# Optimization experiments

Measured on AMD Instinct MI355X. Metric: run time of the kernel, lower is better.

Reference implementation:

```python
import jax, jax.numpy as jnp
import numpy as np

# --- fixed OpenCV filter kernels ---
# cv2.getGaussianKernel(3, 1): exp(-(i-1)^2/2), normalized -> [0.27407, 0.45186, 0.27407]
_g = np.exp(-((np.arange(3) - 1.0) ** 2) / 2.0)
GAUSS_1D = (_g / _g.sum()).astype(np.float32)
# cv2 Sobel/Laplacian ksize=9 separable parts (unnormalized, as cv2.Laplacian uses):
#   smoothing = binomial row C(8,k); second derivative = C(6,k) conv [1,-2,1]
SMOOTH_9 = np.array([1, 8, 28, 56, 70, 56, 28, 8, 1], dtype=np.float32)
D2_9 = np.array([1, 4, 4, -4, -10, -4, 4, 4, 1], dtype=np.float32)


def _depthwise_conv(x, k2d):
    """Depthwise 2D correlation with BORDER_REFLECT_101 padding (cv2 default).

    x: [N,H,W,C] float, k2d: [kh,kw] float (symmetric, so corr == conv)."""
    C = x.shape[-1]
    rh, rw = k2d.shape[0] // 2, k2d.shape[1] // 2
    # jnp 'reflect' == OpenCV BORDER_REFLECT_101 (edge pixel not duplicated)
    xp = jnp.pad(x, ((0, 0), (rh, rh), (rw, rw), (0, 0)), mode='reflect')
    k = jnp.broadcast_to(k2d[:, :, None, None], (k2d.shape[0], k2d.shape[1], 1, C))
    return jax.lax.conv_general_dilated(
        xp, k, window_strides=(1, 1), padding='VALID',
        dimension_numbers=('NHWC', 'HWIO', 'NHWC'),
        feature_group_count=C)


def setup_inputs() -> dict:
    key = jax.random.key(0)
    # uint8-range image batch, as the original layer feeds uint8 data to OpenCV
    x = jax.random.uniform(key, (32, 512, 512, 3), dtype=jnp.float32) * 255.0
    return {"x": x}


def reference(x) -> jnp.ndarray:
    g = jnp.asarray(GAUSS_1D)
    blur = _depthwise_conv(x, jnp.outer(g, g))  # GaussianBlur(ksize=3, sigma=1)
    lap_k = jnp.asarray(np.outer(SMOOTH_9, D2_9) + np.outer(D2_9, SMOOTH_9))
    lap = _depthwise_conv(blur, lap_k) + 1.0  # delta = 1
    # CV_8UC1 destination depth -> saturate to [0, 255]
    return jnp.clip(lap, 0.0, 255.0)
```

## Files before the change

### kernel.cpp

```cpp
#include <hip/hip_runtime.h>


#define TH 16
#define TW 32
#define BF ((TW+8)*3)
#define PH (TH+2)
#define VW 124
#define PW 108
#define HIMG 512
#define WIMG 512
#define ROWF (WIMG*3)

#define OFF_VQ 3120
#define SM_TOTAL 5352

__device__ __forceinline__ int reflect101(int i, int n) {
    i = (i < 0) ? -i : i;
    return (i >= n) ? (2 * n - 2 - i) : i;
}

__device__ __forceinline__ float4 fma4(float s, const float4& a, const float4& b) {
    return make_float4(fmaf(s, a.x, b.x), fmaf(s, a.y, b.y),
                       fmaf(s, a.z, b.z), fmaf(s, a.w, b.w));
}

__device__ __forceinline__ float c6dot(float f0, float f1, float f2, float f3,
                                       float f4, float f5, float f6) {
    return fmaf(20.f, f3, fmaf(6.f, f1 + f5, fmaf(15.f, f2 + f4, f0 + f6)));
}

__device__ __forceinline__ float4 g3(const float4& a, const float4& b, const float4& c,
                                     float G0, float G1) {
    return make_float4(G0 * (a.x + c.x) + G1 * b.x,
                       G0 * (a.y + c.y) + G1 * b.y,
                       G0 * (a.z + c.z) + G1 * b.z,
                       G0 * (a.w + c.w) + G1 * b.w);
}

#define U0 0.27406862f
#define U1 2.09627447f
#define U2 7.09627447f
#define U3 13.90372553f
#define U4 17.25931382f

__global__ __launch_bounds__(256, 6)
void log_fused(const float* __restrict__ x, float* __restrict__ out) {
    __shared__ __align__(16) float smem[SM_TOTAL];
    float* const hblur = smem;
    float* const P     = smem;
    float* const vq    = smem + OFF_VQ;

    const int tid  = threadIdx.x;
    const int col0 = blockIdx.x * TW;
    const int row0 = blockIdx.y * TH;
    const int n    = blockIdx.z;

    const int R0    = max(0, row0 - 5);
    const int R1    = min(HIMG - 1, row0 + TH + 4);
    const int nrows = R1 - R0 + 1;

    const float G0 = 0.2740686190f, G1 = 0.4518627620f;

    if (tid < PH)
        *(float4*)&vq[tid * VW + 120] = make_float4(0.f, 0.f, 0.f, 0.f);

    const bool edgecol = (col0 == 0) || (col0 + TW == WIMG);
    if (!edgecol) {
        if (tid < 240) {
            const int cg = tid % 30;
            const int rg = tid / 30;
            const float* xb = x + ((size_t)n * HIMG + (size_t)(R0 + rg)) * ROWF
                                + (3 * (col0 - 4) + 4 * cg - 4);
            float* hb = hblur + rg * BF + 4 * cg;
            for (int r = rg; r < nrows; r += 8, xb += 8 * ROWF, hb += 8 * BF) {
                const float4 a = *(const float4*)(xb);
                const float4 b = *(const float4*)(xb + 4);
                const float4 c = *(const float4*)(xb + 8);
                float4 o;
                o.x = G0 * (a.y + b.w) + G1 * b.x;
                o.y = G0 * (a.z + c.x) + G1 * b.y;
                o.z = G0 * (a.w + c.y) + G1 * b.z;
                o.w = G0 * (b.x + c.z) + G1 * b.w;
                *(float4*)hb = o;
            }
        }
    } else {
        if (tid < 240) {
            const int lc  = tid % BF;
            const int rg  = tid / BF;
            const int lcp = lc / 3;
            const int ch  = lc - 3 * lcp;
            const int gc  = reflect101(col0 - 4 + lcp, WIMG);
            const int xm  = reflect101(gc - 1, WIMG) * 3 + ch;
            const int x0  = gc * 3 + ch;
            const int xp  = reflect101(gc + 1, WIMG) * 3 + ch;
            const float* xr = x + ((size_t)n * HIMG + (size_t)(R0 + rg)) * ROWF;
            for (int r = rg; r < nrows; r += 2, xr += 2 * ROWF) {
                hblur[r * BF + lc] = G0 * (xr[xm] + xr[xp]) + G1 * xr[x0];
            }
        }
    }
    __syncthreads();

    if (row0 != 0 && row0 != HIMG - TH) {
        if (tid < 180) {
            const int rg = tid / 30;
            const int qc = tid % 30;
            const float U9k[9] = {U0, U1, U2, U3, U4, U3, U2, U1, U0};
            const float* hb = hblur + (3 * rg) * BF + 4 * qc;
            float4 a0 = make_float4(0.f, 0.f, 0.f, 0.f), a1 = a0, a2 = a0;
            #pragma unroll
            for (int j = 0; j < 11; ++j) {
                const float4 w = *(const float4*)(hb + j * BF);
                if (j <= 8)           a0 = fma4(U9k[j],     w, a0);
                if (j >= 1 && j <= 9) a1 = fma4(U9k[j - 1], w, a1);
                if (j >= 2)           a2 = fma4(U9k[j - 2], w, a2);
            }
            float* vp = vq + (3 * rg) * VW + 4 * qc;
            *(float4*)vp            = a0;
            *(float4*)(vp + VW)     = a1;
            *(float4*)(vp + 2 * VW) = a2;
        }
    } else {
        const float C6k[7] = {1.f, 6.f, 15.f, 20.f, 15.f, 6.f, 1.f};
        for (int g = tid; g < PH * 30; g += 256) {
            const int r  = g / 30;
            const int qc = g - r * 30;
            const int gb = row0 - 4 + r;
            float4 acc = make_float4(0.f, 0.f, 0.f, 0.f);
            #pragma unroll
            for (int k = 0; k < 7; ++k) {
                const int y  = reflect101(gb + k, HIMG);
                const int ym = reflect101(y - 1, HIMG) - R0;
                const int yp = reflect101(y + 1, HIMG) - R0;
                const float4 a = *(const float4*)&hblur[ym * BF + 4 * qc];
                const float4 b = *(const float4*)&hblur[(y - R0) * BF + 4 * qc];
                const float4 c = *(const float4*)&hblur[yp * BF + 4 * qc];
                acc = fma4(C6k[k], g3(a, b, c, G0, G1), acc);
            }
            *(float4*)&vq[r * VW + 4 * qc] = acc;
        }
    }
    __syncthreads();

    if (tid < PH * 13) {
        const int qp = tid % 13;
        const int r  = tid / 13;
        const float* v = vq + r * VW + 8 * qp;
        float f[28];
        #pragma unroll
        for (int c = 0; c < 7; ++c) {
            const float4 w = *(const float4*)(v + 4 * c);
            f[4*c+0] = w.x; f[4*c+1] = w.y; f[4*c+2] = w.z; f[4*c+3] = w.w;
        }
        float p[8];
        #pragma unroll
        for (int j = 0; j < 8; ++j)
            p[j] = c6dot(f[j], f[j+3], f[j+6], f[j+9], f[j+12], f[j+15], f[j+18]);
        float* pr = P + r * PW + 8 * qp;
        *(float4*)pr       = make_float4(p[0], p[1], p[2], p[3]);
        *(float4*)(pr + 4) = make_float4(p[4], p[5], p[6], p[7]);
    }
    __syncthreads();

    float* const outn = out + (size_t)n * HIMG * ROWF;
    if (tid < TH * 12) {
        const int qp = tid % 12;
        const int i  = tid / 12;
        const int o  = qp * 8;
        const float* pt = P + i * PW + o;
        const float* pm = pt + PW;
        const float* pb = pm + PW;
        float t[16], m[12], b[16];
        #pragma unroll
        for (int q = 0; q < 4; ++q) {
            const float4 vt = *(const float4*)(pt + 4 * q);
            t[4*q+0] = vt.x; t[4*q+1] = vt.y; t[4*q+2] = vt.z; t[4*q+3] = vt.w;
            const float4 vb = *(const float4*)(pb + 4 * q);
            b[4*q+0] = vb.x; b[4*q+1] = vb.y; b[4*q+2] = vb.z; b[4*q+3] = vb.w;
        }
        #pragma unroll
        for (int q = 0; q < 3; ++q) {
            const float4 vm = *(const float4*)(pm + 4 * q);
            m[4*q+0] = vm.x; m[4*q+1] = vm.y; m[4*q+2] = vm.z; m[4*q+3] = vm.w;
        }
        float o8[8];
        #pragma unroll
        for (int j = 0; j < 8; ++j) {
            const float c = m[j + 3];
            const float s = (t[j] - c) + (t[j + 6] - c) + (b[j] - c) + (b[j + 6] - c);
            const float v = fmaf(2.f, s, 1.f);
            o8[j] = fminf(fmaxf(v, 0.f), 255.f);
        }
        float* op = outn + (size_t)(row0 + i) * ROWF + (size_t)(col0 * 3 + o);
        *(float4*)op       = make_float4(o8[0], o8[1], o8[2], o8[3]);
        *(float4*)(op + 4) = make_float4(o8[4], o8[5], o8[6], o8[7]);
    }
}

extern "C" void kernel_launch(void* const* d_in, const int* in_sizes, int n_in,
                              void* d_out, int out_size, void* d_ws, size_t ws_size,
                              hipStream_t stream) {
    const float* x = (const float*)d_in[0];
    float* outp = (float*)d_out;
    const int nimg = in_sizes[0] / (HIMG * WIMG * 3);
    dim3 grid(WIMG / TW, HIMG / TH, nimg);
    log_fused<<<grid, dim3(256, 1, 1), 0, stream>>>(x, outp);
}
```

Before: 221.7 us.

## Double tile height, software-pipeline row loads, vectorize edge-column blur path

```diff
diff --git a/kernel.cpp b/kernel.cpp
--- a/kernel.cpp
+++ b/kernel.cpp
@@ -1,9 +1,9 @@
 #include <hip/hip_runtime.h>
 
 
-#define TH 16
+#define TH 32
 #define TW 32
-#define BF ((TW+8)*3)
+#define BF 120
 #define PH (TH+2)
 #define VW 124
 #define PW 108
@@ -11,8 +11,8 @@
 #define WIMG 512
 #define ROWF (WIMG*3)
 
-#define OFF_VQ 3120
-#define SM_TOTAL 5352
+#define OFF_VQ 5040
+#define SM_TOTAL 9256
 
 __device__ __forceinline__ int reflect101(int i, int n) {
     i = (i < 0) ? -i : i;
@@ -27,14 +27,6 @@
 __device__ __forceinline__ float c6dot(float f0, float f1, float f2, float f3,
                                        float f4, float f5, float f6) {
     return fmaf(20.f, f3, fmaf(6.f, f1 + f5, fmaf(15.f, f2 + f4, f0 + f6)));
-}
-
-__device__ __forceinline__ float4 g3(const float4& a, const float4& b, const float4& c,
-                                     float G0, float G1) {
-    return make_float4(G0 * (a.x + c.x) + G1 * b.x,
-                       G0 * (a.y + c.y) + G1 * b.y,
-                       G0 * (a.z + c.z) + G1 * b.z,
-                       G0 * (a.w + c.w) + G1 * b.w);
 }
 
 #define U0 0.27406862f
@@ -43,7 +35,7 @@
 #define U3 13.90372553f
 #define U4 17.25931382f
 
-__global__ __launch_bounds__(256, 6)
+__global__ __launch_bounds__(256, 4)
 void log_fused(const float* __restrict__ x, float* __restrict__ out) {
     __shared__ __align__(16) float smem[SM_TOTAL];
     float* const hblur = smem;
@@ -54,6 +46,7 @@
     const int col0 = blockIdx.x * TW;
     const int row0 = blockIdx.y * TH;
     const int n    = blockIdx.z;
+    const float* const xi = x + (size_t)n * HIMG * ROWF;
 
     const int R0    = max(0, row0 - 5);
     const int R1    = min(HIMG - 1, row0 + TH + 4);
@@ -69,45 +62,79 @@
         if (tid < 240) {
             const int cg = tid % 30;
             const int rg = tid / 30;
-            const float* xb = x + ((size_t)n * HIMG + (size_t)(R0 + rg)) * ROWF
-                                + (3 * (col0 - 4) + 4 * cg - 4);
+            const float* xp = xi + (size_t)(R0 + rg) * ROWF
+                                 + (3 * (col0 - 4) + 4 * cg - 4);
             float* hb = hblur + rg * BF + 4 * cg;
-            for (int r = rg; r < nrows; r += 8, xb += 8 * ROWF, hb += 8 * BF) {
-                const float4 a = *(const float4*)(xb);
-                const float4 b = *(const float4*)(xb + 4);
-                const float4 c = *(const float4*)(xb + 8);
+            int r = rg;
+            float4 A0 = *(const float4*)(xp);
+            float4 A1 = *(const float4*)(xp + 4);
+            float4 A2 = *(const float4*)(xp + 8);
+            while (true) {
+                const int rn = r + 8;
+                const bool hn = rn < nrows;
+                const float* xn = xp + 8 * ROWF;
+                float4 B0, B1, B2;
+                if (hn) {
+                    B0 = *(const float4*)(xn);
+                    B1 = *(const float4*)(xn + 4);
+                    B2 = *(const float4*)(xn + 8);
+                }
                 float4 o;
+                o.x = G0 * (A0.y + A1.w) + G1 * A1.x;
+                o.y = G0 * (A0.z + A2.x) + G1 * A1.y;
+                o.z = G0 * (A0.w + A2.y) + G1 * A1.z;
+                o.w = G0 * (A1.x + A2.z) + G1 * A1.w;
+                *(float4*)hb = o;
+                if (!hn) break;
+                A0 = B0; A1 = B1; A2 = B2;
+                r = rn; xp = xn; hb += 8 * BF;
+            }
+        }
+    } else {
+        for (int e = tid; e < nrows * 30; e += 256) {
+            const int row = e / 30;
+            const int q   = e - row * 30;
+            const float* xr = xi + (size_t)(R0 + row) * ROWF;
+            const int lcpmin = (4 * q) / 3;
+            const int lcpmax = (4 * q + 3) / 3;
+            const bool safe = (col0 - 5 + lcpmin >= 0) && (col0 - 3 + lcpmax <= WIMG - 1);
+            float4 o;
+            if (safe) {
+                const float* p = xr + (3 * col0 - 16 + 4 * q);
+                const float4 a = *(const float4*)(p);
+                const float4 b = *(const float4*)(p + 4);
+                const float4 c = *(const float4*)(p + 8);
                 o.x = G0 * (a.y + b.w) + G1 * b.x;
                 o.y = G0 * (a.z + c.x) + G1 * b.y;
                 o.z = G0 * (a.w + c.y) + G1 * b.z;
                 o.w = G0 * (b.x + c.z) + G1 * b.w;
-                *(float4*)hb = o;
-            }
-        }
-    } else {
-        if (tid < 240) {
-            const int lc  = tid % BF;
-            const int rg  = tid / BF;
-            const int lcp = lc / 3;
-            const int ch  = lc - 3 * lcp;
-            const int gc  = reflect101(col0 - 4 + lcp, WIMG);
-            const int xm  = reflect101(gc - 1, WIMG) * 3 + ch;
-            const int x0  = gc * 3 + ch;
-            const int xp  = reflect101(gc + 1, WIMG) * 3 + ch;
-            const float* xr = x + ((size_t)n * HIMG + (size_t)(R0 + rg)) * ROWF;
-            for (int r = rg; r < nrows; r += 2, xr += 2 * ROWF) {
-                hblur[r * BF + lc] = G0 * (xr[xm] + xr[xp]) + G1 * xr[x0];
-            }
+            } else {
+                float t[4];
+                #pragma unroll
+                for (int m = 0; m < 4; ++m) {
+                    const int lc  = 4 * q + m;
+                    const int lcp = lc / 3;
+                    const int ch  = lc - 3 * lcp;
+                    const int gc  = reflect101(col0 - 4 + lcp, WIMG);
+                    const int xm  = reflect101(gc - 1, WIMG) * 3 + ch;
+                    const int x0  = gc * 3 + ch;
+                    const int xp2 = reflect101(gc + 1, WIMG) * 3 + ch;
+                    t[m] = G0 * (xr[xm] + xr[xp2]) + G1 * xr[x0];
+                }
+                o = make_float4(t[0], t[1], t[2], t[3]);
+            }
+            *(float4*)&hblur[row * BF + 4 * q] = o;
         }
     }
     __syncthreads();
 
     if (row0 != 0 && row0 != HIMG - TH) {
-        if (tid < 180) {
-            const int rg = tid / 30;
-            const int qc = tid % 30;
-            const float U9k[9] = {U0, U1, U2, U3, U4, U3, U2, U1, U0};
-            const float* hb = hblur + (3 * rg) * BF + 4 * qc;
+        const float U9k[9] = {U0, U1, U2, U3, U4, U3, U2, U1, U0};
+        for (int g = tid; g < 360; g += 256) {
+            const int tg = g / 30;
+            const int qc = g - tg * 30;
+            const int s  = min(3 * tg, PH - 3);
+            const float* hb = hblur + s * BF + 4 * qc;
             float4 a0 = make_float4(0.f, 0.f, 0.f, 0.f), a1 = a0, a2 = a0;
             #pragma unroll
             for (int j = 0; j < 11; ++j) {
@@ -116,7 +143,7 @@
                 if (j >= 1 && j <= 9) a1 = fma4(U9k[j - 1], w, a1);
                 if (j >= 2)           a2 = fma4(U9k[j - 2], w, a2);
             }
-            float* vp = vq + (3 * rg) * VW + 4 * qc;
+            float* vp = vq + s * VW + 4 * qc;
             *(float4*)vp            = a0;
             *(float4*)(vp + VW)     = a1;
             *(float4*)(vp + 2 * VW) = a2;
@@ -136,16 +163,20 @@
                 const float4 a = *(const float4*)&hblur[ym * BF + 4 * qc];
                 const float4 b = *(const float4*)&hblur[(y - R0) * BF + 4 * qc];
                 const float4 c = *(const float4*)&hblur[yp * BF + 4 * qc];
-                acc = fma4(C6k[k], g3(a, b, c, G0, G1), acc);
+                const float4 gg = make_float4(G0 * (a.x + c.x) + G1 * b.x,
+                                              G0 * (a.y + c.y) + G1 * b.y,
+                                              G0 * (a.z + c.z) + G1 * b.z,
+                                              G0 * (a.w + c.w) + G1 * b.w);
+                acc = fma4(C6k[k], gg, acc);
             }
             *(float4*)&vq[r * VW + 4 * qc] = acc;
         }
     }
     __syncthreads();
 
-    if (tid < PH * 13) {
-        const int qp = tid % 13;
-        const int r  = tid / 13;
+    for (int g = tid; g < PH * 13; g += 256) {
+        const int r  = g / 13;
+        const int qp = g - r * 13;
         const float* v = vq + r * VW + 8 * qp;
         float f[28];
         #pragma unroll
@@ -164,9 +195,9 @@
     __syncthreads();
 
     float* const outn = out + (size_t)n * HIMG * ROWF;
-    if (tid < TH * 12) {
-        const int qp = tid % 12;
-        const int i  = tid / 12;
+    for (int g = tid; g < TH * 12; g += 256) {
+        const int i  = g / 12;
+        const int qp = g - i * 12;
         const int o  = qp * 8;
         const float* pt = P + i * PW + o;
         const float* pm = pt + PW;
```

Result: slower. 244.4 us (+10.2%).
